# Kernel optimization log

Hardware: AMD Instinct MI355X
Metric: run time of the kernel (lower is better)

The kernel has to match this reference:

```python
import jax, jax.numpy as jnp
import numpy as np

N, E, G, C, H, O = 100000, 600000, 1000, 2, 128, 10
HC = H // 2  # cls MLP hidden

def _bn(x, g, b, rm, rv):
    # eval-mode BatchNorm1d with running stats
    return (x - rm) * jax.lax.rsqrt(rv + 1e-5) * g + b

def setup_inputs() -> dict:
    key = jax.random.key(0)
    ks = iter(jax.random.split(key, 64))
    rn = lambda shape, s=0.05: jax.random.normal(next(ks), shape, jnp.float32) * s
    inp = {
        'pos': jax.random.normal(next(ks), (N, C), jnp.float32),
        'edge_index': jax.random.randint(next(ks), (2, E), 0, N),
        'batch': jnp.sort(jax.random.randint(next(ks), (N,), 0, G)),
    }
    def bn_params(pfx):
        return {pfx+'g': jnp.ones((H,), jnp.float32), pfx+'b': jnp.zeros((H,), jnp.float32),
                pfx+'rm': rn((H,)), pfx+'rv': jax.random.uniform(next(ks), (H,), jnp.float32, 0.5, 1.5)}
    # conv1 nn: Lin(C,H)-ReLU-Lin(H,H)-ReLU-BN
    inp.update(W1a=rn((C, H)), b1a=jnp.zeros((H,)), W1b=rn((H, H)), b1b=jnp.zeros((H,)))
    inp.update(bn_params('n1_'))
    # conv2 nn: Lin(H,H)-ReLU-Lin(H,H)-ReLU-BN
    inp.update(W2a=rn((H, H)), b2a=jnp.zeros((H,)), W2b=rn((H, H)), b2b=jnp.zeros((H,)))
    inp.update(bn_params('n2_'))
    # fc1: Lin(C,H)-ReLU-BN ; fc2: Lin(H,H)-ReLU-BN (weights SHARED for both fc2 calls)
    inp.update(Wf1=rn((C, H)), bf1=jnp.zeros((H,)))
    inp.update(bn_params('f1_'))
    inp.update(Wf2=rn((H, H)), bf2=jnp.zeros((H,)))
    inp.update(bn_params('f2_'))
    # cls MLP: Lin(H,HC)-BN-PReLU-Lin(HC,O)
    inp.update(Wc1=rn((H, HC)), bc1=jnp.zeros((HC,)),
               gc=jnp.ones((HC,), jnp.float32), bec=jnp.zeros((HC,), jnp.float32),
               rmc=rn((HC,)), rvc=jax.random.uniform(next(ks), (HC,), jnp.float32, 0.5, 1.5),
               a_prelu=jnp.asarray(0.25, jnp.float32),
               Wc2=rn((HC, O)), bc2=jnp.zeros((O,)))
    return inp


def reference(pos, edge_index, batch,
              W1a, b1a, W1b, b1b, n1_g, n1_b, n1_rm, n1_rv,
              W2a, b2a, W2b, b2b, n2_g, n2_b, n2_rm, n2_rv,
              Wf1, bf1, f1_g, f1_b, f1_rm, f1_rv,
              Wf2, bf2, f2_g, f2_b, f2_rm, f2_rv,
              Wc1, bc1, gc, bec, rmc, rvc, a_prelu, Wc2, bc2):
    src, dst = edge_index[0], edge_index[1]

    def gin_nn(h, Wa, ba, Wb, bb, g, b, rm, rv):
        h = jax.nn.relu(h @ Wa + ba)
        h = jax.nn.relu(h @ Wb + bb)
        return _bn(h, g, b, rm, rv)

    def gin(x, Wa, ba, Wb, bb, g, b, rm, rv):
        # GINConv, eps=0: nn((1+eps)*x + sum_{j in N(i)} x_j)
        agg = jax.ops.segment_sum(x[src], dst, num_segments=N)
        return gin_nn(x + agg, Wa, ba, Wb, bb, g, b, rm, rv)

    def fc(x, W, b, g, be, rm, rv):
        return _bn(jax.nn.relu(x @ W + b), g, be, rm, rv)

    pool = lambda h: jax.ops.segment_sum(h, batch, num_segments=G)

    x0_g = fc(pool(pos), Wf1, bf1, f1_g, f1_b, f1_rm, f1_rv)           # [G,H]
    x1 = gin(pos, W1a, b1a, W1b, b1b, n1_g, n1_b, n1_rm, n1_rv)        # [N,H]
    x1_g = fc(x0_g + pool(x1), Wf2, bf2, f2_g, f2_b, f2_rm, f2_rv)     # [G,H]
    x2 = gin(x1, W2a, b2a, W2b, b2b, n2_g, n2_b, n2_rm, n2_rv)         # [N,H]
    x2_g = fc(x0_g + x1_g + pool(x2), Wf2, bf2, f2_g, f2_b, f2_rm, f2_rv)

    # dropout inactive in eval; cls MLP with PReLU
    h = x2_g @ Wc1 + bc1
    h = _bn(h, gc, bec, rmc, rvc)
    h = jnp.where(h > 0, h, a_prelu * h)
    return h @ Wc2 + bc2  # [G,O]
```

## Files before the change

kernel.cpp:

```cpp
#include <hip/hip_runtime.h>

#define H 128
#define HC 64
#define NOUT 10

static constexpr int kN = 100000;
static constexpr int kE = 600000;
static constexpr int kG = 1000;

typedef __attribute__((ext_vector_type(8))) short short8v;
typedef __attribute__((ext_vector_type(4))) float f32x4;

__device__ __forceinline__ float4 ld4(const float* p) { return *(const float4*)p; }

__device__ __forceinline__ unsigned f2bf(float f) {
    unsigned u = __float_as_uint(f);
    return (u + 0x7fffu + ((u >> 16) & 1u)) >> 16;
}
__device__ __forceinline__ unsigned f2bf2(float a, float b) {
    return f2bf(a) | (f2bf(b) << 16);
}
__device__ __forceinline__ float bf2f(unsigned short u) {
    return __uint_as_float(((unsigned)u) << 16);
}
__device__ __forceinline__ void unpack_add8(uint4 u, float* a) {
    a[0] += __uint_as_float(u.x << 16); a[1] += __uint_as_float(u.x & 0xFFFF0000u);
    a[2] += __uint_as_float(u.y << 16); a[3] += __uint_as_float(u.y & 0xFFFF0000u);
    a[4] += __uint_as_float(u.z << 16); a[5] += __uint_as_float(u.z & 0xFFFF0000u);
    a[6] += __uint_as_float(u.w << 16); a[7] += __uint_as_float(u.w & 0xFFFF0000u);
}

__device__ __forceinline__ int swzmask(int rl) { return (rl & 15) << 3; }

__global__ void k_setup(int* __restrict__ deg,
                        const float* __restrict__ Wa, const float* __restrict__ Wb,
                        const float* __restrict__ Wc, unsigned short* __restrict__ wpk,
                        const int* __restrict__ batch, int* __restrict__ browptr) {
    int gt = blockIdx.x * blockDim.x + threadIdx.x;
    if (gt < 25000) {
        ((int4*)deg)[gt] = make_int4(0, 0, 0, 0);
    } else if (gt < 25000 + 6144) {
        int gt2 = gt - 25000;
        int m = gt2 >> 11, t = gt2 & 2047;
        const float* W = (m == 0) ? Wa : (m == 1) ? Wb : Wc;
        int lane = t & 63, fc = t >> 6;
        int kb = fc >> 3, c16 = fc & 7;
        int col = c16 * 16 + (lane & 15);
        int k0 = kb * 32 + (lane >> 4) * 8;
        unsigned r[4];
#pragma unroll
        for (int p = 0; p < 4; ++p) {
            float a = W[(size_t)(k0 + 2 * p) * H + col];
            float b = W[(size_t)(k0 + 2 * p + 1) * H + col];
            r[p] = f2bf2(a, b);
        }
        *(uint4*)(wpk + (size_t)m * 16384 + (size_t)t * 8) = make_uint4(r[0], r[1], r[2], r[3]);
    } else if (gt < 25000 + 6144 + kG + 1) {
        int g = gt - (25000 + 6144);
        int lo = 0, hi = kN;
        while (lo < hi) {
            int mid = (lo + hi) >> 1;
            if (batch[mid] < g) lo = mid + 1; else hi = mid;
        }
        browptr[g] = lo;
    }
}

__global__ void k_hist(const int* __restrict__ keys, int* __restrict__ cnt, int n) {
    int i = blockIdx.x * blockDim.x + threadIdx.x;
    if (i < n) atomicAdd(&cnt[keys[i]], 1);
}

__global__ void k_scan_p1(const int* __restrict__ in, int* __restrict__ partial, int n) {
    __shared__ int red[256];
    int b = blockIdx.x, t = threadIdx.x;
    int base = b * 1024 + t * 4;
    int s = 0;
#pragma unroll
    for (int k = 0; k < 4; ++k) {
        int j = base + k;
        if (j < n) s += in[j];
    }
    red[t] = s;
    __syncthreads();
    for (int off = 128; off; off >>= 1) {
        if (t < off) red[t] += red[t + off];
        __syncthreads();
    }
    if (t == 0) partial[b] = red[0];
}

__global__ void k_scan_p2(int* __restrict__ partial, int* __restrict__ total_out, int nb) {
    __shared__ int ssum[1024];
    int t = threadIdx.x;
    int v = (t < nb) ? partial[t] : 0;
    ssum[t] = v;
    __syncthreads();
    for (int off = 1; off < 1024; off <<= 1) {
        int u = (t >= off) ? ssum[t - off] : 0;
        __syncthreads();
        ssum[t] += u;
        __syncthreads();
    }
    if (t < nb) partial[t] = ssum[t] - v;
    if (t == 1023 && total_out) *total_out = ssum[1023];
}

__global__ void k_scan_p3(const int* __restrict__ in, const int* __restrict__ partial,
                          int* __restrict__ out, int* __restrict__ cursor, int n) {
    __shared__ int red[256];
    int b = blockIdx.x, t = threadIdx.x;
    int base = b * 1024 + t * 4;
    int v[4];
    int s = 0;
#pragma unroll
    for (int k = 0; k < 4; ++k) {
        int j = base + k;
        v[k] = (j < n) ? in[j] : 0;
        s += v[k];
    }
    red[t] = s;
    __syncthreads();
    for (int off = 1; off < 256; off <<= 1) {
        int u = (t >= off) ? red[t - off] : 0;
        __syncthreads();
        red[t] += u;
        __syncthreads();
    }
    int tbase = partial[b] + red[t] - s;
#pragma unroll
    for (int k = 0; k < 4; ++k) {
        int j = base + k;
        if (j < n) {
            out[j] = tbase;
            if (cursor) cursor[j] = tbase;
            tbase += v[k];
        }
    }
}

__global__ void k_scatter(const int* __restrict__ src, const int* __restrict__ dst,
                          int* __restrict__ cursor, int* __restrict__ eidx, int E) {
    int e = blockIdx.x * blockDim.x + threadIdx.x;
    if (e >= E) return;
    int slot = atomicAdd(&cursor[dst[e]], 1);
    eidx[slot] = src[e];
}

__global__ void k_gather_add(const int* __restrict__ rowptr, const int* __restrict__ eidx,
                             const unsigned short* __restrict__ x, unsigned short* __restrict__ out,
                             int nN) {
    int idx = blockIdx.x * blockDim.x + threadIdx.x;
    int i = idx >> 4, q = idx & 15;
    if (i >= nN) return;
    const int off = q * 8;
    float a[8] = {0, 0, 0, 0, 0, 0, 0, 0};
    unpack_add8(*(const uint4*)(x + (size_t)i * H + off), a);
    int j0 = rowptr[i], j1 = rowptr[i + 1];
    for (int j = j0; j < j1; ++j) {
        int s = eidx[j];
        unpack_add8(*(const uint4*)(x + (size_t)s * H + off), a);
    }
    *(uint4*)(out + (size_t)i * H + off) =
        make_uint4(f2bf2(a[0], a[1]), f2bf2(a[2], a[3]), f2bf2(a[4], a[5]), f2bf2(a[6], a[7]));
}

__global__ __launch_bounds__(256) void k_gin1(
    const float* __restrict__ pos,
    const int* __restrict__ rowptr, const int* __restrict__ eidx,
    const float* __restrict__ W1a, const float* __restrict__ b1a,
    const short8v* __restrict__ wpk, const float* __restrict__ bias,
    const float* __restrict__ bn_g, const float* __restrict__ bn_b,
    const float* __restrict__ bn_rm, const float* __restrict__ bn_rv,
    unsigned short* __restrict__ out, int nN) {
    __shared__ unsigned short As[H * H];
    __shared__ float sB[H], sS[H], sH2[H];
    const int t = threadIdx.x;

    if (t < H) {
        sB[t] = bias[t];
        float s = bn_g[t] * rsqrtf(bn_rv[t] + 1e-5f);
        sS[t] = s;
        sH2[t] = bn_b[t] - bn_rm[t] * s;
    }

    {
        const int rl = t >> 1, half = t & 1;
        const int ic = min(blockIdx.x * 128 + rl, nN - 1);
        float2 p = ((const float2*)pos)[ic];
        float x0 = p.x, x1 = p.y;
        int j0 = rowptr[ic], j1 = rowptr[ic + 1];
        for (int j = j0; j < j1; ++j) {
            float2 q = ((const float2*)pos)[eidx[j]];
            x0 += q.x; x1 += q.y;
        }
        const int mask = swzmask(rl);
#pragma unroll
        for (int c4 = 0; c4 < 16; ++c4) {
            int c = half * 64 + c4 * 4;
            float4 w0 = ld4(&W1a[c]);
            float4 w1 = ld4(&W1a[H + c]);
            float4 bb = ld4(&b1a[c]);
            float r0 = fmaxf(x0 * w0.x + x1 * w1.x + bb.x, 0.f);
            float r1 = fmaxf(x0 * w0.y + x1 * w1.y + bb.y, 0.f);
            float r2 = fmaxf(x0 * w0.z + x1 * w1.z + bb.z, 0.f);
            float r3 = fmaxf(x0 * w0.w + x1 * w1.w + bb.w, 0.f);
            int idx = rl * H + c;
            *(uint2*)(As + (idx ^ mask)) = make_uint2(f2bf2(r0, r1), f2bf2(r2, r3));
        }
    }
    __syncthreads();

    const int lane = t & 63;
    const int wave = t >> 6;
    const int rowbase = blockIdx.x * 128 + wave * 32;
    const int lrow = lane & 15;
    const int lhi = lane >> 4;

    f32x4 acc[2][8];
#pragma unroll
    for (int rr = 0; rr < 2; ++rr)
#pragma unroll
        for (int c = 0; c < 8; ++c) acc[rr][c] = (f32x4){0.f, 0.f, 0.f, 0.f};

#pragma unroll
    for (int kb = 0; kb < 4; ++kb) {
        short8v xf[2];
#pragma unroll
        for (int rr = 0; rr < 2; ++rr) {
            int rl = wave * 32 + rr * 16 + lrow;
            int idx = rl * H + kb * 32 + lhi * 8;
            xf[rr] = *(const short8v*)(As + (idx ^ swzmask(rl)));
        }
#pragma unroll
        for (int c16 = 0; c16 < 8; ++c16) {
            short8v wf = wpk[(kb * 8 + c16) * 64 + lane];
            acc[0][c16] = __builtin_amdgcn_mfma_f32_16x16x32_bf16(wf, xf[0], acc[0][c16], 0, 0, 0);
            acc[1][c16] = __builtin_amdgcn_mfma_f32_16x16x32_bf16(wf, xf[1], acc[1][c16], 0, 0, 0);
        }
    }

#pragma unroll
    for (int c16 = 0; c16 < 8; ++c16) {
        const int c0 = c16 * 16 + lhi * 4;
        float b0 = sB[c0], b1 = sB[c0 + 1], b2 = sB[c0 + 2], b3 = sB[c0 + 3];
        float s0 = sS[c0], s1 = sS[c0 + 1], s2 = sS[c0 + 2], s3 = sS[c0 + 3];
        float h0 = sH2[c0], h1 = sH2[c0 + 1], h2 = sH2[c0 + 2], h3 = sH2[c0 + 3];
#pragma unroll
        for (int rr = 0; rr < 2; ++rr) {
            int row = rowbase + rr * 16 + lrow;
            if (row >= nN) continue;
            float v0 = fmaxf(acc[rr][c16][0] + b0, 0.f) * s0 + h0;
            float v1 = fmaxf(acc[rr][c16][1] + b1, 0.f) * s1 + h1;
            float v2 = fmaxf(acc[rr][c16][2] + b2, 0.f) * s2 + h2;
            float v3 = fmaxf(acc[rr][c16][3] + b3, 0.f) * s3 + h3;
            *(uint2*)(out + (size_t)row * H + c0) = make_uint2(f2bf2(v0, v1), f2bf2(v2, v3));
        }
    }
}

__global__ __launch_bounds__(256) void k_gin2(
    const unsigned short* __restrict__ xin, const short8v* __restrict__ wpA,
    const float* __restrict__ biasA, const short8v* __restrict__ wpB,
    const float* __restrict__ biasB,
    const float* __restrict__ bn_g, const float* __restrict__ bn_b,
    const float* __restrict__ bn_rm, const float* __restrict__ bn_rv,
    unsigned short* __restrict__ out, int nN) {
    __shared__ unsigned short As[H * H];
    __shared__ float sBa[H], sBb[H], sS[H], sH2[H];
    const int t = threadIdx.x;

    if (t < H) {
        sBa[t] = biasA[t];
        sBb[t] = biasB[t];
        float s = bn_g[t] * rsqrtf(bn_rv[t] + 1e-5f);
        sS[t] = s;
        sH2[t] = bn_b[t] - bn_rm[t] * s;
    }
    __syncthreads();

    const int lane = t & 63;
    const int wave = t >> 6;
    const int rowbase = blockIdx.x * 128 + wave * 32;
    const int lrow = lane & 15;
    const int lhi = lane >> 4;

    f32x4 acc[2][8];
#pragma unroll
    for (int rr = 0; rr < 2; ++rr)
#pragma unroll
        for (int c = 0; c < 8; ++c) acc[rr][c] = (f32x4){0.f, 0.f, 0.f, 0.f};

#pragma unroll
    for (int kb = 0; kb < 4; ++kb) {
        short8v xf[2];
#pragma unroll
        for (int rr = 0; rr < 2; ++rr) {
            int row = rowbase + rr * 16 + lrow;
            row = row < nN ? row : nN - 1;
            xf[rr] = *(const short8v*)(xin + (size_t)row * H + kb * 32 + lhi * 8);
        }
#pragma unroll
        for (int c16 = 0; c16 < 8; ++c16) {
            short8v wf = wpA[(kb * 8 + c16) * 64 + lane];
            acc[0][c16] = __builtin_amdgcn_mfma_f32_16x16x32_bf16(wf, xf[0], acc[0][c16], 0, 0, 0);
            acc[1][c16] = __builtin_amdgcn_mfma_f32_16x16x32_bf16(wf, xf[1], acc[1][c16], 0, 0, 0);
        }
    }

#pragma unroll
    for (int c16 = 0; c16 < 8; ++c16) {
        const int c0 = c16 * 16 + lhi * 4;
        float b0 = sBa[c0], b1 = sBa[c0 + 1], b2 = sBa[c0 + 2], b3 = sBa[c0 + 3];
#pragma unroll
        for (int rr = 0; rr < 2; ++rr) {
            int rl = wave * 32 + rr * 16 + lrow;
            float v0 = fmaxf(acc[rr][c16][0] + b0, 0.f);
            float v1 = fmaxf(acc[rr][c16][1] + b1, 0.f);
            float v2 = fmaxf(acc[rr][c16][2] + b2, 0.f);
            float v3 = fmaxf(acc[rr][c16][3] + b3, 0.f);
            int idx = rl * H + c0;
            *(uint2*)(As + (idx ^ swzmask(rl))) = make_uint2(f2bf2(v0, v1), f2bf2(v2, v3));
        }
    }
    __syncthreads();

#pragma unroll
    for (int rr = 0; rr < 2; ++rr)
#pragma unroll
        for (int c = 0; c < 8; ++c) acc[rr][c] = (f32x4){0.f, 0.f, 0.f, 0.f};

#pragma unroll
    for (int kb = 0; kb < 4; ++kb) {
        short8v xf[2];
#pragma unroll
        for (int rr = 0; rr < 2; ++rr) {
            int rl = wave * 32 + rr * 16 + lrow;
            int idx = rl * H + kb * 32 + lhi * 8;
            xf[rr] = *(const short8v*)(As + (idx ^ swzmask(rl)));
        }
#pragma unroll
        for (int c16 = 0; c16 < 8; ++c16) {
            short8v wf = wpB[(kb * 8 + c16) * 64 + lane];
            acc[0][c16] = __builtin_amdgcn_mfma_f32_16x16x32_bf16(wf, xf[0], acc[0][c16], 0, 0, 0);
            acc[1][c16] = __builtin_amdgcn_mfma_f32_16x16x32_bf16(wf, xf[1], acc[1][c16], 0, 0, 0);
        }
    }

#pragma unroll
    for (int c16 = 0; c16 < 8; ++c16) {
        const int c0 = c16 * 16 + lhi * 4;
        float b0 = sBb[c0], b1 = sBb[c0 + 1], b2 = sBb[c0 + 2], b3 = sBb[c0 + 3];
        float s0 = sS[c0], s1 = sS[c0 + 1], s2 = sS[c0 + 2], s3 = sS[c0 + 3];
        float h0 = sH2[c0], h1 = sH2[c0 + 1], h2 = sH2[c0 + 2], h3 = sH2[c0 + 3];
#pragma unroll
        for (int rr = 0; rr < 2; ++rr) {
            int row = rowbase + rr * 16 + lrow;
            if (row >= nN) continue;
            float v0 = fmaxf(acc[rr][c16][0] + b0, 0.f) * s0 + h0;
            float v1 = fmaxf(acc[rr][c16][1] + b1, 0.f) * s1 + h1;
            float v2 = fmaxf(acc[rr][c16][2] + b2, 0.f) * s2 + h2;
            float v3 = fmaxf(acc[rr][c16][3] + b3, 0.f) * s3 + h3;
            *(uint2*)(out + (size_t)row * H + c0) = make_uint2(f2bf2(v0, v1), f2bf2(v2, v3));
        }
    }
}

__global__ void k_graph(const float* __restrict__ pos,
                        const unsigned short* __restrict__ x1, const unsigned short* __restrict__ x2,
                        const int* __restrict__ browptr,
                        const float* __restrict__ Wf1, const float* __restrict__ bf1,
                        const float* __restrict__ f1g, const float* __restrict__ f1b,
                        const float* __restrict__ f1rm, const float* __restrict__ f1rv,
                        const float* __restrict__ Wf2, const float* __restrict__ bf2,
                        const float* __restrict__ f2g, const float* __restrict__ f2b,
                        const float* __restrict__ f2rm, const float* __restrict__ f2rv,
                        const float* __restrict__ Wc1, const float* __restrict__ bc1,
                        const float* __restrict__ gc, const float* __restrict__ bec,
                        const float* __restrict__ rmc, const float* __restrict__ rvc,
                        const float* __restrict__ ap,
                        const float* __restrict__ Wc2, const float* __restrict__ bc2,
                        float* __restrict__ out) {
    __shared__ float sx[H], sy[H], row[H], hbuf[HC];
    const int gi = blockIdx.x, t = threadIdx.x;
    const int r0 = browptr[gi], r1 = browptr[gi + 1];

    float ax = 0.f, ay = 0.f;
    for (int r = r0 + t; r < r1; r += H) {
        float2 p = ((const float2*)pos)[r];
        ax += p.x; ay += p.y;
    }
    sx[t] = ax; sy[t] = ay;
    __syncthreads();
    for (int off = 64; off; off >>= 1) {
        if (t < off) { sx[t] += sx[t + off]; sy[t] += sy[t + off]; }
        __syncthreads();
    }
    float px = sx[0], py = sy[0];

    float a0 = fmaxf(bf1[t] + px * Wf1[t] + py * Wf1[H + t], 0.f);
    float s1v = f1g[t] * rsqrtf(f1rv[t] + 1e-5f);
    float x0 = (a0 - f1rm[t]) * s1v + f1b[t];

    float p1 = 0.f, p2 = 0.f;
    for (int r = r0; r < r1; ++r) {
        p1 += bf2f(x1[(size_t)r * H + t]);
        p2 += bf2f(x2[(size_t)r * H + t]);
    }

    const float s2v = f2g[t] * rsqrtf(f2rv[t] + 1e-5f);

    row[t] = p1 + x0;
    __syncthreads();
    float a = bf2[t];
    for (int j = 0; j < H; ++j) a += row[j] * Wf2[j * H + t];
    float x1gv = (fmaxf(a, 0.f) - f2rm[t]) * s2v + f2b[t];
    __syncthreads();

    row[t] = p2 + x0 + x1gv;
    __syncthreads();
    a = bf2[t];
    for (int j = 0; j < H; ++j) a += row[j] * Wf2[j * H + t];
    float x2gv = (fmaxf(a, 0.f) - f2rm[t]) * s2v + f2b[t];
    __syncthreads();
    row[t] = x2gv;
    __syncthreads();

    if (t < HC) {
        float c = bc1[t];
        for (int j = 0; j < H; ++j) c += row[j] * Wc1[j * HC + t];
        float sc = gc[t] * rsqrtf(rvc[t] + 1e-5f);
        c = (c - rmc[t]) * sc + bec[t];
        float al = ap[0];
        hbuf[t] = c > 0.f ? c : al * c;
    }
    __syncthreads();
    if (t < NOUT) {
        float c = bc2[t];
        for (int j = 0; j < HC; ++j) c += hbuf[j] * Wc2[j * NOUT + t];
        out[gi * NOUT + t] = c;
    }
}

extern "C" void kernel_launch(void* const* d_in, const int* in_sizes, int n_in,
                              void* d_out, int out_size, void* d_ws, size_t ws_size,
                              hipStream_t stream) {
    const int N = kN, E = kE, G = kG;
    const float* pos = (const float*)d_in[0];
    const int* ei    = (const int*)d_in[1];
    const int* batch = (const int*)d_in[2];
    const float* W1a = (const float*)d_in[3];
    const float* b1a = (const float*)d_in[4];
    const float* W1b = (const float*)d_in[5];
    const float* b1b = (const float*)d_in[6];
    const float* n1g = (const float*)d_in[7];
    const float* n1b = (const float*)d_in[8];
    const float* n1rm = (const float*)d_in[9];
    const float* n1rv = (const float*)d_in[10];
    const float* W2a = (const float*)d_in[11];
    const float* b2a = (const float*)d_in[12];
    const float* W2b = (const float*)d_in[13];
    const float* b2b = (const float*)d_in[14];
    const float* n2g = (const float*)d_in[15];
    const float* n2b = (const float*)d_in[16];
    const float* n2rm = (const float*)d_in[17];
    const float* n2rv = (const float*)d_in[18];
    const float* Wf1 = (const float*)d_in[19];
    const float* bf1 = (const float*)d_in[20];
    const float* f1g = (const float*)d_in[21];
    const float* f1b = (const float*)d_in[22];
    const float* f1rm = (const float*)d_in[23];
    const float* f1rv = (const float*)d_in[24];
    const float* Wf2 = (const float*)d_in[25];
    const float* bf2 = (const float*)d_in[26];
    const float* f2g = (const float*)d_in[27];
    const float* f2b = (const float*)d_in[28];
    const float* f2rm = (const float*)d_in[29];
    const float* f2rv = (const float*)d_in[30];
    const float* Wc1 = (const float*)d_in[31];
    const float* bc1 = (const float*)d_in[32];
    const float* gc  = (const float*)d_in[33];
    const float* bec = (const float*)d_in[34];
    const float* rmc = (const float*)d_in[35];
    const float* rvc = (const float*)d_in[36];
    const float* ap  = (const float*)d_in[37];
    const float* Wc2 = (const float*)d_in[38];
    const float* bc2 = (const float*)d_in[39];
    float* out = (float*)d_out;

    unsigned short* bx1 = (unsigned short*)d_ws;
    unsigned short* bx2 = bx1 + (size_t)N * H;
    unsigned short* wp  = bx2 + (size_t)N * H;
    int* deg     = (int*)(wp + 3 * 16384);
    int* rowptr  = deg + N;
    int* browptr = rowptr + N + 1;
    int* partial = browptr + G + 1;
    int* eidx    = partial + 1024;

    const short8v* wp1 = (const short8v*)wp;
    const short8v* wp2 = (const short8v*)(wp + 16384);
    const short8v* wp3 = (const short8v*)(wp + 32768);

    const int* src  = ei;
    const int* dstp = ei + E;
    const int nb = (N + 1023) / 1024;

    k_setup<<<126, 256, 0, stream>>>(deg, W1b, W2a, W2b, wp, batch, browptr);
    k_hist<<<(E + 255) / 256, 256, 0, stream>>>(dstp, deg, E);
    k_scan_p1<<<nb, 256, 0, stream>>>(deg, partial, N);
    k_scan_p2<<<1, 1024, 0, stream>>>(partial, rowptr + N, nb);
    k_scan_p3<<<nb, 256, 0, stream>>>(deg, partial, rowptr, deg, N);
    k_scatter<<<(E + 255) / 256, 256, 0, stream>>>(src, dstp, deg, eidx, E);

    const int mmBlocks = (N + 127) / 128;

    k_gin1<<<mmBlocks, 256, 0, stream>>>(pos, rowptr, eidx, W1a, b1a, wp1, b1b,
                                         n1g, n1b, n1rm, n1rv, bx1, N);
    k_gather_add<<<(N * 16 + 255) / 256, 256, 0, stream>>>(rowptr, eidx, bx1, bx2, N);
    k_gin2<<<mmBlocks, 256, 0, stream>>>(bx2, wp2, b2a, wp3, b2b,
                                         n2g, n2b, n2rm, n2rv, bx2, N);
    k_graph<<<G, H, 0, stream>>>(pos, bx1, bx2, browptr,
                                 Wf1, bf1, f1g, f1b, f1rm, f1rv,
                                 Wf2, bf2, f2g, f2b, f2rm, f2rv,
                                 Wc1, bc1, gc, bec, rmc, rvc, ap, Wc2, bc2, out);
}
```

Measured before the change: 233.9 us.

## Parallelize graph pooling over rows, transpose FC weights, fold scan pass into p3

The per-graph kernel now runs 256 threads and splits each graph's rows across 16 row-lanes, with each lane loading 16-byte bf16 vectors and reducing through shuffles and shared memory. Before, a single thread walked every row of a graph serially. The Wf2 and Wc1 weights are transposed in the setup kernel so the small matvecs read contiguous float4 rows. The single-block k_scan_p2 launch is removed, and each scan_p3 block computes its own prefix from the partial sums. This saves one launch at the cost of redundant small reductions and a larger setup kernel.

```diff
diff --git a/kernel.cpp b/kernel.cpp
--- a/kernel.cpp
+++ b/kernel.cpp
@@ -19,9 +19,6 @@
 }
 __device__ __forceinline__ unsigned f2bf2(float a, float b) {
     return f2bf(a) | (f2bf(b) << 16);
-}
-__device__ __forceinline__ float bf2f(unsigned short u) {
-    return __uint_as_float(((unsigned)u) << 16);
 }
 __device__ __forceinline__ void unpack_add8(uint4 u, float* a) {
     a[0] += __uint_as_float(u.x << 16); a[1] += __uint_as_float(u.x & 0xFFFF0000u);
@@ -35,11 +32,13 @@
 __global__ void k_setup(int* __restrict__ deg,
                         const float* __restrict__ Wa, const float* __restrict__ Wb,
                         const float* __restrict__ Wc, unsigned short* __restrict__ wpk,
-                        const int* __restrict__ batch, int* __restrict__ browptr) {
+                        const int* __restrict__ batch, int* __restrict__ browptr,
+                        const float* __restrict__ Wf2, float* __restrict__ Wf2T,
+                        const float* __restrict__ Wc1, float* __restrict__ Wc1T) {
     int gt = blockIdx.x * blockDim.x + threadIdx.x;
     if (gt < 25000) {
         ((int4*)deg)[gt] = make_int4(0, 0, 0, 0);
-    } else if (gt < 25000 + 6144) {
+    } else if (gt < 31144) {
         int gt2 = gt - 25000;
         int m = gt2 >> 11, t = gt2 & 2047;
         const float* W = (m == 0) ? Wa : (m == 1) ? Wb : Wc;
@@ -55,14 +54,32 @@
             r[p] = f2bf2(a, b);
         }
         *(uint4*)(wpk + (size_t)m * 16384 + (size_t)t * 8) = make_uint4(r[0], r[1], r[2], r[3]);
-    } else if (gt < 25000 + 6144 + kG + 1) {
-        int g = gt - (25000 + 6144);
+    } else if (gt < 32145) {
+        int g = gt - 31144;
         int lo = 0, hi = kN;
         while (lo < hi) {
             int mid = (lo + hi) >> 1;
             if (batch[mid] < g) lo = mid + 1; else hi = mid;
         }
         browptr[g] = lo;
+    } else if (gt < 36241) {
+        int id = gt - 32145;
+        int col = id >> 5, j4 = id & 31;
+        float4 v;
+        v.x = Wf2[(j4 * 4 + 0) * H + col];
+        v.y = Wf2[(j4 * 4 + 1) * H + col];
+        v.z = Wf2[(j4 * 4 + 2) * H + col];
+        v.w = Wf2[(j4 * 4 + 3) * H + col];
+        ((float4*)Wf2T)[col * 32 + j4] = v;
+    } else if (gt < 38289) {
+        int id = gt - 36241;
+        int t64 = id >> 5, j4 = id & 31;
+        float4 v;
+        v.x = Wc1[(j4 * 4 + 0) * HC + t64];
+        v.y = Wc1[(j4 * 4 + 1) * HC + t64];
+        v.z = Wc1[(j4 * 4 + 2) * HC + t64];
+        v.w = Wc1[(j4 * 4 + 3) * HC + t64];
+        ((float4*)Wc1T)[t64 * 32 + j4] = v;
     }
 }
 
@@ -90,26 +107,19 @@
     if (t == 0) partial[b] = red[0];
 }
 
-__global__ void k_scan_p2(int* __restrict__ partial, int* __restrict__ total_out, int nb) {
-    __shared__ int ssum[1024];
-    int t = threadIdx.x;
-    int v = (t < nb) ? partial[t] : 0;
-    ssum[t] = v;
-    __syncthreads();
-    for (int off = 1; off < 1024; off <<= 1) {
-        int u = (t >= off) ? ssum[t - off] : 0;
-        __syncthreads();
-        ssum[t] += u;
-        __syncthreads();
-    }
-    if (t < nb) partial[t] = ssum[t] - v;
-    if (t == 1023 && total_out) *total_out = ssum[1023];
-}
-
 __global__ void k_scan_p3(const int* __restrict__ in, const int* __restrict__ partial,
-                          int* __restrict__ out, int* __restrict__ cursor, int n) {
+                          int* __restrict__ out, int* __restrict__ cursor, int n, int nb) {
+    __shared__ int bb[256];
     __shared__ int red[256];
     int b = blockIdx.x, t = threadIdx.x;
+    bb[t] = (t < b) ? partial[t] : 0;
+    __syncthreads();
+    for (int off = 128; off; off >>= 1) {
+        if (t < off) bb[t] += bb[t + off];
+        __syncthreads();
+    }
+    int bbase = bb[0];
+
     int base = b * 1024 + t * 4;
     int v[4];
     int s = 0;
@@ -127,7 +137,7 @@
         red[t] += u;
         __syncthreads();
     }
-    int tbase = partial[b] + red[t] - s;
+    int tbase = bbase + red[t] - s;
 #pragma unroll
     for (int k = 0; k < 4; ++k) {
         int j = base + k;
@@ -137,6 +147,7 @@
             tbase += v[k];
         }
     }
+    if (b == nb - 1 && t == 255) out[n] = bbase + red[255];
 }
 
 __global__ void k_scatter(const int* __restrict__ src, const int* __restrict__ dst,
@@ -366,69 +377,117 @@
     }
 }
 
-__global__ void k_graph(const float* __restrict__ pos,
-                        const unsigned short* __restrict__ x1, const unsigned short* __restrict__ x2,
-                        const int* __restrict__ browptr,
-                        const float* __restrict__ Wf1, const float* __restrict__ bf1,
-                        const float* __restrict__ f1g, const float* __restrict__ f1b,
-                        const float* __restrict__ f1rm, const float* __restrict__ f1rv,
-                        const float* __restrict__ Wf2, const float* __restrict__ bf2,
-                        const float* __restrict__ f2g, const float* __restrict__ f2b,
-                        const float* __restrict__ f2rm, const float* __restrict__ f2rv,
-                        const float* __restrict__ Wc1, const float* __restrict__ bc1,
-                        const float* __restrict__ gc, const float* __restrict__ bec,
-                        const float* __restrict__ rmc, const float* __restrict__ rvc,
-                        const float* __restrict__ ap,
-                        const float* __restrict__ Wc2, const float* __restrict__ bc2,
-                        float* __restrict__ out) {
-    __shared__ float sx[H], sy[H], row[H], hbuf[HC];
+__global__ __launch_bounds__(256) void k_graph(
+    const float* __restrict__ pos,
+    const unsigned short* __restrict__ x1, const unsigned short* __restrict__ x2,
+    const int* __restrict__ browptr,
+    const float* __restrict__ Wf1, const float* __restrict__ bf1,
+    const float* __restrict__ f1g, const float* __restrict__ f1b,
+    const float* __restrict__ f1rm, const float* __restrict__ f1rv,
+    const float* __restrict__ Wf2T, const float* __restrict__ bf2,
+    const float* __restrict__ f2g, const float* __restrict__ f2b,
+    const float* __restrict__ f2rm, const float* __restrict__ f2rv,
+    const float* __restrict__ Wc1T, const float* __restrict__ bc1,
+    const float* __restrict__ gc, const float* __restrict__ bec,
+    const float* __restrict__ rmc, const float* __restrict__ rvc,
+    const float* __restrict__ ap,
+    const float* __restrict__ Wc2, const float* __restrict__ bc2,
+    float* __restrict__ out) {
+    __shared__ float redx[256], redy[256];
+    __shared__ float part1[4][16][8], part2[4][16][8];
+    __shared__ float row[H];
+    __shared__ float hbuf[HC];
     const int gi = blockIdx.x, t = threadIdx.x;
     const int r0 = browptr[gi], r1 = browptr[gi + 1];
 
     float ax = 0.f, ay = 0.f;
-    for (int r = r0 + t; r < r1; r += H) {
+    for (int r = r0 + t; r < r1; r += 256) {
         float2 p = ((const float2*)pos)[r];
         ax += p.x; ay += p.y;
     }
-    sx[t] = ax; sy[t] = ay;
-    __syncthreads();
-    for (int off = 64; off; off >>= 1) {
-        if (t < off) { sx[t] += sx[t + off]; sy[t] += sy[t + off]; }
+    redx[t] = ax; redy[t] = ay;
+    __syncthreads();
+    for (int off = 128; off; off >>= 1) {
+        if (t < off) { redx[t] += redx[t + off]; redy[t] += redy[t + off]; }
         __syncthreads();
     }
-    float px = sx[0], py = sy[0];
-
-    float a0 = fmaxf(bf1[t] + px * Wf1[t] + py * Wf1[H + t], 0.f);
-    float s1v = f1g[t] * rsqrtf(f1rv[t] + 1e-5f);
-    float x0 = (a0 - f1rm[t]) * s1v + f1b[t];
-
-    float p1 = 0.f, p2 = 0.f;
-    for (int r = r0; r < r1; ++r) {
-        p1 += bf2f(x1[(size_t)r * H + t]);
-        p2 += bf2f(x2[(size_t)r * H + t]);
-    }
-
-    const float s2v = f2g[t] * rsqrtf(f2rv[t] + 1e-5f);
-
-    row[t] = p1 + x0;
-    __syncthreads();
-    float a = bf2[t];
-    for (int j = 0; j < H; ++j) a += row[j] * Wf2[j * H + t];
-    float x1gv = (fmaxf(a, 0.f) - f2rm[t]) * s2v + f2b[t];
-    __syncthreads();
-
-    row[t] = p2 + x0 + x1gv;
-    __syncthreads();
-    a = bf2[t];
-    for (int j = 0; j < H; ++j) a += row[j] * Wf2[j * H + t];
-    float x2gv = (fmaxf(a, 0.f) - f2rm[t]) * s2v + f2b[t];
-    __syncthreads();
-    row[t] = x2gv;
+    const float px = redx[0], py = redy[0];
+
+    {
+        const int c = t & 15, l = t >> 4;
+        float a1[8] = {0, 0, 0, 0, 0, 0, 0, 0};
+        float a2[8] = {0, 0, 0, 0, 0, 0, 0, 0};
+        for (int r = r0 + l; r < r1; r += 16) {
+            unpack_add8(*(const uint4*)(x1 + (size_t)r * H + c * 8), a1);
+            unpack_add8(*(const uint4*)(x2 + (size_t)r * H + c * 8), a2);
+        }
+#pragma unroll
+        for (int k = 0; k < 8; ++k) {
+            a1[k] += __shfl_xor(a1[k], 16); a1[k] += __shfl_xor(a1[k], 32);
+            a2[k] += __shfl_xor(a2[k], 16); a2[k] += __shfl_xor(a2[k], 32);
+        }
+        const int wv = t >> 6, lane = t & 63;
+        if (lane < 16) {
+#pragma unroll
+            for (int k = 0; k < 8; ++k) {
+                part1[wv][lane][k] = a1[k];
+                part2[wv][lane][k] = a2[k];
+            }
+        }
+    }
+    __syncthreads();
+
+    float x0 = 0.f, p1 = 0.f, p2 = 0.f, s2v = 0.f;
+    if (t < H) {
+        const int cc = t >> 3, e = t & 7;
+        p1 = part1[0][cc][e] + part1[1][cc][e] + part1[2][cc][e] + part1[3][cc][e];
+        p2 = part2[0][cc][e] + part2[1][cc][e] + part2[2][cc][e] + part2[3][cc][e];
+        float a0 = fmaxf(bf1[t] + px * Wf1[t] + py * Wf1[H + t], 0.f);
+        float s1v = f1g[t] * rsqrtf(f1rv[t] + 1e-5f);
+        x0 = (a0 - f1rm[t]) * s1v + f1b[t];
+        s2v = f2g[t] * rsqrtf(f2rv[t] + 1e-5f);
+        row[t] = p1 + x0;
+    }
+    __syncthreads();
+
+    float x1gv = 0.f;
+    if (t < H) {
+        float a = bf2[t];
+        const float4* wt = (const float4*)(Wf2T + t * H);
+#pragma unroll 8
+        for (int j4 = 0; j4 < 32; ++j4) {
+            float4 w = wt[j4];
+            a += row[j4 * 4] * w.x + row[j4 * 4 + 1] * w.y + row[j4 * 4 + 2] * w.z + row[j4 * 4 + 3] * w.w;
+        }
+        x1gv = (fmaxf(a, 0.f) - f2rm[t]) * s2v + f2b[t];
+    }
+    __syncthreads();
+    if (t < H) row[t] = p2 + x0 + x1gv;
+    __syncthreads();
+
+    float x2gv = 0.f;
+    if (t < H) {
+        float a = bf2[t];
+        const float4* wt = (const float4*)(Wf2T + t * H);
+#pragma unroll 8
+        for (int j4 = 0; j4 < 32; ++j4) {
+            float4 w = wt[j4];
+            a += row[j4 * 4] * w.x + row[j4 * 4 + 1] * w.y + row[j4 * 4 + 2] * w.z + row[j4 * 4 + 3] * w.w;
+        }
+        x2gv = (fmaxf(a, 0.f) - f2rm[t]) * s2v + f2b[t];
+    }
+    __syncthreads();
+    if (t < H) row[t] = x2gv;
     __syncthreads();
 
     if (t < HC) {
         float c = bc1[t];
-        for (int j = 0; j < H; ++j) c += row[j] * Wc1[j * HC + t];
+        const float4* wt = (const float4*)(Wc1T + t * H);
+#pragma unroll 8
+        for (int j4 = 0; j4 < 32; ++j4) {
+            float4 w = wt[j4];
+            c += row[j4 * 4] * w.x + row[j4 * 4 + 1] * w.y + row[j4 * 4 + 2] * w.z + row[j4 * 4 + 3] * w.w;
+        }
         float sc = gc[t] * rsqrtf(rvc[t] + 1e-5f);
         c = (c - rmc[t]) * sc + bec[t];
         float al = ap[0];
@@ -491,7 +550,9 @@
     unsigned short* bx1 = (unsigned short*)d_ws;
     unsigned short* bx2 = bx1 + (size_t)N * H;
     unsigned short* wp  = bx2 + (size_t)N * H;
-    int* deg     = (int*)(wp + 3 * 16384);
+    float* wf2t  = (float*)(wp + 3 * 16384);
+    float* wc1t  = wf2t + 16384;
+    int* deg     = (int*)(wc1t + 8192);
     int* rowptr  = deg + N;
     int* browptr = rowptr + N + 1;
     int* partial = browptr + G + 1;
@@ -505,11 +566,11 @@
     const int* dstp = ei + E;
     const int nb = (N + 1023) / 1024;
 
-    k_setup<<<126, 256, 0, stream>>>(deg, W1b, W2a, W2b, wp, batch, browptr);
+    k_setup<<<150, 256, 0, stream>>>(deg, W1b, W2a, W2b, wp, batch, browptr,
+                                     Wf2, wf2t, Wc1, wc1t);
     k_hist<<<(E + 255) / 256, 256, 0, stream>>>(dstp, deg, E);
     k_scan_p1<<<nb, 256, 0, stream>>>(deg, partial, N);
-    k_scan_p2<<<1, 1024, 0, stream>>>(partial, rowptr + N, nb);
-    k_scan_p3<<<nb, 256, 0, stream>>>(deg, partial, rowptr, deg, N);
+    k_scan_p3<<<nb, 256, 0, stream>>>(deg, partial, rowptr, deg, N, nb);
     k_scatter<<<(E + 255) / 256, 256, 0, stream>>>(src, dstp, deg, eidx, E);
 
     const int mmBlocks = (N + 127) / 128;
@@ -519,8 +580,8 @@
     k_gather_add<<<(N * 16 + 255) / 256, 256, 0, stream>>>(rowptr, eidx, bx1, bx2, N);
     k_gin2<<<mmBlocks, 256, 0, stream>>>(bx2, wp2, b2a, wp3, b2b,
                                          n2g, n2b, n2rm, n2rv, bx2, N);
-    k_graph<<<G, H, 0, stream>>>(pos, bx1, bx2, browptr,
-                                 Wf1, bf1, f1g, f1b, f1rm, f1rv,
-                                 Wf2, bf2, f2g, f2b, f2rm, f2rv,
-                                 Wc1, bc1, gc, bec, rmc, rvc, ap, Wc2, bc2, out);
-}
+    k_graph<<<G, 256, 0, stream>>>(pos, bx1, bx2, browptr,
+                                   Wf1, bf1, f1g, f1b, f1rm, f1rv,
+                                   wf2t, bf2, f2g, f2b, f2rm, f2rv,
+                                   wc1t, bc1, gc, bec, rmc, rvc, ap, Wc2, bc2, out);
+}
```

Measured after the change: 214.3 us. -8.4%, faster.
